# Performance work log

Hardware: AMD Instinct MI355X
Metric: run time of the kernel (lower is better)

Reference implementation:

```python
import jax, jax.numpy as jnp
import numpy as np

H, W = 128, 128
TANFOVX = 0.5
TANFOVY = 0.5
SCALE_MOD = 1.0
NEAR = 0.2
N = 2048


def setup_inputs() -> dict:
    key = jax.random.key(0)
    ks = jax.random.split(key, 6)
    # Gaussians in front of an identity camera looking down +z
    xy = jax.random.uniform(ks[0], (N, 2), minval=-1.5, maxval=1.5)
    z = jax.random.uniform(ks[1], (N, 1), minval=2.5, maxval=6.5)
    means3D = jnp.concatenate([xy, z], axis=1).astype(jnp.float32)
    opacities = jax.random.uniform(ks[2], (N, 1), minval=0.05, maxval=0.95)
    colors_precomp = jax.random.uniform(ks[3], (N, 3))
    scales = jax.random.uniform(ks[4], (N, 3), minval=0.01, maxval=0.06)
    rotations = jax.random.normal(ks[5], (N, 4))
    viewmatrix = jnp.eye(4, dtype=jnp.float32)  # world == camera frame
    bg = jnp.zeros((3,), dtype=jnp.float32)
    return dict(means3D=means3D, opacities=opacities,
                colors_precomp=colors_precomp, scales=scales,
                rotations=rotations, viewmatrix=viewmatrix, bg=bg)


def _quat_to_rot(q):
    # normalized quaternion (w, x, y, z) -> rotation matrix, as in the CUDA kernel
    q = q / jnp.linalg.norm(q, axis=-1, keepdims=True)
    w, x, y, z = q[:, 0], q[:, 1], q[:, 2], q[:, 3]
    return jnp.stack([
        jnp.stack([1 - 2 * (y * y + z * z), 2 * (x * y - w * z), 2 * (x * z + w * y)], -1),
        jnp.stack([2 * (x * y + w * z), 1 - 2 * (x * x + z * z), 2 * (y * z - w * x)], -1),
        jnp.stack([2 * (x * z - w * y), 2 * (y * z + w * x), 1 - 2 * (x * x + y * y)], -1),
    ], -2)  # [N,3,3]


def _forward(means3D, opacities, colors_precomp, scales, rotations, viewmatrix, bg):
    fx = W / (2.0 * TANFOVX)
    fy = H / (2.0 * TANFOVY)
    Rv = viewmatrix[:3, :3]
    tv = viewmatrix[:3, 3]
    pv = means3D @ Rv.T + tv            # view-space positions [N,3]
    x, y, z = pv[:, 0], pv[:, 1], pv[:, 2]
    zc = jnp.maximum(z, 1e-4)
    # frustum clamping of the EWA Jacobian, as in forward.cu
    tx = jnp.clip(x / zc, -1.3 * TANFOVX, 1.3 * TANFOVX) * zc
    ty = jnp.clip(y / zc, -1.3 * TANFOVY, 1.3 * TANFOVY) * zc
    zeros = jnp.zeros_like(zc)
    J = jnp.stack([
        jnp.stack([fx / zc, zeros, -fx * tx / (zc * zc)], -1),
        jnp.stack([zeros, fy / zc, -fy * ty / (zc * zc)], -1),
    ], -2)                               # [N,2,3]
    # 3D covariance Sigma = R S S^T R^T
    Rg = _quat_to_rot(rotations)
    M = Rg * (scales * SCALE_MOD)[:, None, :]
    Sigma = M @ jnp.swapaxes(M, -1, -2)  # [N,3,3]
    T2 = jnp.einsum('nij,jk->nik', J, Rv)
    cov2d = jnp.einsum('nij,njk,nlk->nil', T2, Sigma, T2)
    a = cov2d[:, 0, 0] + 0.3             # low-pass filter, as in CUDA
    b = cov2d[:, 0, 1]
    c = cov2d[:, 1, 1] + 0.3
    det = a * c - b * b
    valid = (det > 0) & (z > NEAR)
    inv_det = jnp.where(det != 0, 1.0 / det, 0.0)
    conA, conB, conC = c * inv_det, -b * inv_det, a * inv_det
    mid = 0.5 * (a + c)
    lam = mid + jnp.sqrt(jnp.maximum(mid * mid - det, 0.1))
    radii = jnp.where(valid, jnp.ceil(3.0 * jnp.sqrt(lam)), 0.0)
    # projected pixel-space means
    mx = fx * (x / zc) + 0.5 * (W - 1)
    my = fy * (y / zc) + 0.5 * (H - 1)

    # global front-to-back depth sort (CUDA sorts per tile; one tile here)
    order = jnp.argsort(z)
    mx_s, my_s = mx[order], my[order]
    A_s, B_s, C_s = conA[order], conB[order], conC[order]
    op_s = opacities[order, 0]
    z_s = z[order]
    col_s = colors_precomp[order]
    valid_s = valid[order]

    px = jnp.arange(W, dtype=means3D.dtype)
    py = jnp.arange(H, dtype=means3D.dtype)
    Dx = mx_s[None, :] - px[:, None]     # [W,N]
    Dy = my_s[None, :] - py[:, None]     # [H,N]
    # power = -0.5 (A dx^2 + C dy^2) - B dx dy, built [H,W,N]
    power = (-0.5 * A_s * Dx * Dx)[None, :, :] \
            + (-0.5 * C_s * Dy * Dy)[:, None, :] \
            - (B_s * Dx)[None, :, :] * Dy[:, None, :]
    alpha = jnp.minimum(0.99, op_s * jnp.exp(jnp.minimum(power, 0.0)))
    alpha = jnp.where((power <= 0.0) & valid_s & (alpha >= 1.0 / 255.0), alpha, 0.0)
    alpha = alpha.reshape(H * W, N)      # [HW,N], front-to-back order
    logt = jnp.log1p(-alpha)
    csum = jnp.cumsum(logt, axis=-1)
    T_excl = jnp.exp(csum - logt)        # exclusive transmittance prod_{j<i}(1-a_j)
    wgt = alpha * T_excl                 # compositing weights
    T_final = jnp.exp(csum[:, -1])
    color = jnp.einsum('pn,nc->cp', wgt, col_s).reshape(3, H, W) \
            + T_final.reshape(1, H, W) * bg[:, None, None]
    depth = (wgt * z_s[None, :]).sum(-1).reshape(H, W)
    alpha_img = (1.0 - T_final).reshape(H, W)
    return color, radii, depth, alpha_img


def reference(means3D, opacities, colors_precomp, scales, rotations, viewmatrix, bg):
    return _forward(means3D, opacities, colors_precomp, scales, rotations, viewmatrix, bg)
```

## Files before the change

### kernel.cpp

```cpp
#include <hip/hip_runtime.h>

#define NG    2048
#define IMG_W 128
#define IMG_H 128
#define NPIX  (IMG_W * IMG_H)
#define KCAP  768

struct PRec {
    double mx, my, A, B, C, op, z, r2c;
    float radii;
};

__device__ __forceinline__ void preprocess_g(
    int i,
    const float* __restrict__ means, const float* __restrict__ opac,
    const float* __restrict__ scales, const float* __restrict__ rots,
    const float* __restrict__ vm4, PRec& o)
{
    const double fx = 128.0, fy = 128.0;

    double R00 = vm4[0], R01 = vm4[1], R02 = vm4[2],  t0 = vm4[3];
    double R10 = vm4[4], R11 = vm4[5], R12 = vm4[6],  t1 = vm4[7];
    double R20 = vm4[8], R21 = vm4[9], R22 = vm4[10], t2 = vm4[11];

    double m0 = means[3*i+0], m1 = means[3*i+1], m2 = means[3*i+2];
    double x = R00*m0 + R01*m1 + R02*m2 + t0;
    double y = R10*m0 + R11*m1 + R12*m2 + t1;
    double z = R20*m0 + R21*m1 + R22*m2 + t2;

    double zc   = fmax(z, 1e-4);
    double invz = 1.0 / zc;
    const double limx = 1.3 * 0.5, limy = 1.3 * 0.5;
    double tx = fmin(limx, fmax(-limx, x * invz)) * zc;
    double ty = fmin(limy, fmax(-limy, y * invz)) * zc;

    double J00 = fx * invz, J02 = -fx * tx * invz * invz;
    double J11 = fy * invz, J12 = -fy * ty * invz * invz;

    double qw = rots[4*i+0], qx = rots[4*i+1], qy = rots[4*i+2], qz = rots[4*i+3];
    double qn = 1.0 / sqrt(qw*qw + qx*qx + qy*qy + qz*qz);
    qw *= qn; qx *= qn; qy *= qn; qz *= qn;

    double Rg00 = 1.0 - 2.0*(qy*qy + qz*qz), Rg01 = 2.0*(qx*qy - qw*qz), Rg02 = 2.0*(qx*qz + qw*qy);
    double Rg10 = 2.0*(qx*qy + qw*qz), Rg11 = 1.0 - 2.0*(qx*qx + qz*qz), Rg12 = 2.0*(qy*qz - qw*qx);
    double Rg20 = 2.0*(qx*qz - qw*qy), Rg21 = 2.0*(qy*qz + qw*qx), Rg22 = 1.0 - 2.0*(qx*qx + qy*qy);

    double s0 = scales[3*i+0], s1 = scales[3*i+1], s2 = scales[3*i+2];
    double M00 = Rg00*s0, M01 = Rg01*s1, M02 = Rg02*s2;
    double M10 = Rg10*s0, M11 = Rg11*s1, M12 = Rg12*s2;
    double M20 = Rg20*s0, M21 = Rg21*s1, M22 = Rg22*s2;

    double S00 = M00*M00 + M01*M01 + M02*M02;
    double S01 = M00*M10 + M01*M11 + M02*M12;
    double S02 = M00*M20 + M01*M21 + M02*M22;
    double S11 = M10*M10 + M11*M11 + M12*M12;
    double S12 = M10*M20 + M11*M21 + M12*M22;
    double S22 = M20*M20 + M21*M21 + M22*M22;

    double Ta0 = J00*R00 + J02*R20, Ta1 = J00*R01 + J02*R21, Ta2 = J00*R02 + J02*R22;
    double Tb0 = J11*R10 + J12*R20, Tb1 = J11*R11 + J12*R21, Tb2 = J11*R12 + J12*R22;

    double Ua0 = Ta0*S00 + Ta1*S01 + Ta2*S02;
    double Ua1 = Ta0*S01 + Ta1*S11 + Ta2*S12;
    double Ua2 = Ta0*S02 + Ta1*S12 + Ta2*S22;
    double Ub0 = Tb0*S00 + Tb1*S01 + Tb2*S02;
    double Ub1 = Tb0*S01 + Tb1*S11 + Tb2*S12;
    double Ub2 = Tb0*S02 + Tb1*S12 + Tb2*S22;
    double cov00 = Ua0*Ta0 + Ua1*Ta1 + Ua2*Ta2;
    double cov01 = Ua0*Tb0 + Ua1*Tb1 + Ua2*Tb2;
    double cov11 = Ub0*Tb0 + Ub1*Tb1 + Ub2*Tb2;

    double a = cov00 + 0.3;
    double b = cov01;
    double c = cov11 + 0.3;
    double det = a*c - b*b;
    bool valid = (det > 0.0) && (z > 0.2);
    double inv_det = (det != 0.0) ? (1.0 / det) : 0.0;
    double mid = 0.5 * (a + c);
    double lam = mid + sqrt(fmax(mid*mid - det, 0.1));

    double op = valid ? (double)opac[i] : 0.0;
    double r2c = -1.0;
    if (op > 0.0) {
        double lnterm = log(255.0 * op);
        if (lnterm > 0.0) r2c = 2.0 * lnterm * lam * 1.0001 + 1e-3;
    }

    o.mx  = fx * (x * invz) + 0.5 * (IMG_W - 1);
    o.my  = fy * (y * invz) + 0.5 * (IMG_H - 1);
    o.A   =  c * inv_det;
    o.B   = -b * inv_det;
    o.C   =  a * inv_det;
    o.op  = op;
    o.z   = z;
    o.r2c = r2c;
    o.radii = valid ? (float)ceil(3.0 * sqrt(lam)) : 0.0f;
}

__global__ __launch_bounds__(256) void fused_raster_kernel(
    const float* __restrict__ means,
    const float* __restrict__ opac,
    const float* __restrict__ cols,
    const float* __restrict__ scales,
    const float* __restrict__ rots,
    const float* __restrict__ vm4,
    const float* __restrict__ bg,
    float* __restrict__ out)
{
    __shared__ unsigned short cand[NG];
    __shared__ float recs[KCAP][10];
    __shared__ float pz[KCAP];
    __shared__ unsigned short pid[KCAP];
    __shared__ unsigned short perm[KCAP];
    __shared__ float comb[4 * 64 * 5];
    __shared__ int cntM, cntK;

    int tid  = threadIdx.x;
    int tile = blockIdx.x;
    int x0 = (tile & 15) * 8;
    int y0 = (tile >> 4) * 8;
    float x0f = (float)x0,       y0f = (float)y0;
    float x1f = (float)(x0 + 7), y1f = (float)(y0 + 7);

    if (tid == 0) { cntM = 0; cntK = 0; }
    __syncthreads();

    float fR00 = vm4[0], fR01 = vm4[1], fR02 = vm4[2],  ft0 = vm4[3];
    float fR10 = vm4[4], fR11 = vm4[5], fR12 = vm4[6],  ft1 = vm4[7];
    float fR20 = vm4[8], fR21 = vm4[9], fR22 = vm4[10], ft2 = vm4[11];

    for (int g = tid; g < NG; g += 256) {
        float m0 = means[3*g+0], m1 = means[3*g+1], m2 = means[3*g+2];
        float x = fR00*m0 + fR01*m1 + fR02*m2 + ft0;
        float y = fR10*m0 + fR11*m1 + fR12*m2 + ft1;
        float z = fR20*m0 + fR21*m1 + fR22*m2 + ft2;
        float zc = fmaxf(z, 1e-4f);
        float invz = 1.0f / zc;
        float xi = x * invz, yi = y * invz;
        float mx = 128.f * xi + 63.5f;
        float my = 128.f * yi + 63.5f;
        float txc = fminf(0.65f, fmaxf(-0.65f, xi));
        float tyc = fminf(0.65f, fmaxf(-0.65f, yi));
        float J00 = 128.f * invz;
        float J02 = -128.f * txc * invz;
        float J12 = -128.f * tyc * invz;
        float Ta0 = J00*fR00 + J02*fR20, Ta1 = J00*fR01 + J02*fR21, Ta2 = J00*fR02 + J02*fR22;
        float Tb0 = J00*fR10 + J12*fR20, Tb1 = J00*fR11 + J12*fR21, Tb2 = J00*fR12 + J12*fR22;
        float fro = Ta0*Ta0 + Ta1*Ta1 + Ta2*Ta2 + Tb0*Tb0 + Tb1*Tb1 + Tb2*Tb2;
        float s0 = scales[3*g+0], s1 = scales[3*g+1], s2 = scales[3*g+2];
        float smax2 = fmaxf(s0*s0, fmaxf(s1*s1, s2*s2));
        float op = opac[g];
        float lnterm = __logf(255.f * op);
        bool maybe = false;
        if (lnterm > 0.f) {
            float lam_pf = fro * smax2 * 1.02f + 0.95f;
            float r2 = 2.f * lnterm * lam_pf * 1.02f + 1.0f;
            float ddx = fmaxf(0.f, fmaxf(x0f - mx, mx - x1f));
            float ddy = fmaxf(0.f, fmaxf(y0f - my, my - y1f));
            maybe = (ddx*ddx + ddy*ddy) <= r2;
        }
        if (maybe) {
            int s = atomicAdd(&cntM, 1);
            cand[s] = (unsigned short)g;
        }
    }

    if (tid < 8) {
        int i = tile * 8 + tid;
        PRec o;
        preprocess_g(i, means, opac, scales, rots, vm4, o);
        out[3*NPIX + i] = o.radii;
    }
    __syncthreads();
    int M = cntM;

    for (int k = tid; k < M; k += 256) {
        int gi = cand[k];
        PRec o;
        preprocess_g(gi, means, opac, scales, rots, vm4, o);
        float fmx = (float)o.mx, fmy = (float)o.my, fr2 = (float)o.r2c;
        float ddx = fmaxf(0.f, fmaxf(x0f - fmx, fmx - x1f));
        float ddy = fmaxf(0.f, fmaxf(y0f - fmy, fmy - y1f));
        if (ddx*ddx + ddy*ddy <= fr2) {
            int s = atomicAdd(&cntK, 1);
            if (s < KCAP) {
                recs[s][0] = fmx;
                recs[s][1] = fmy;
                recs[s][2] = (float)o.A;
                recs[s][3] = (float)o.B;
                recs[s][4] = (float)o.C;
                recs[s][5] = (float)o.op;
                recs[s][6] = (float)o.z;
                recs[s][7] = cols[3*gi+0];
                recs[s][8] = cols[3*gi+1];
                recs[s][9] = cols[3*gi+2];
                pz[s]  = (float)o.z;
                pid[s] = (unsigned short)gi;
            }
        }
    }
    __syncthreads();
    int K = min(cntK, KCAP);

    for (int r = tid; r < K; r += 256) {
        float zr = pz[r];
        int ir = pid[r];
        int rank = 0;
        for (int s2 = 0; s2 < K; ++s2)
            rank += (pz[s2] < zr) || (pz[s2] == zr && pid[s2] < ir);
        perm[rank] = (unsigned short)r;
    }
    __syncthreads();

    int lane = tid & 63;
    int w    = tid >> 6;
    int px = x0 + (lane & 7);
    int py = y0 + (lane >> 3);
    float fpx = (float)px, fpy = (float)py;
    int p = py * IMG_W + px;

    int q = (K + 3) >> 2;
    int rs = w * q;
    int re = min(rs + q, K);

    float cr = 0.f, cg = 0.f, cb = 0.f, dep = 0.f, T = 1.f;
    for (int r = rs; r < re; ++r) {
        int j = perm[r];
        float mx = recs[j][0];
        float my = recs[j][1];
        float A  = recs[j][2];
        float B  = recs[j][3];
        float C  = recs[j][4];
        float op = recs[j][5];
        float dx = mx - fpx;
        float dy = my - fpy;
        float power = -0.5f * (A*dx*dx + C*dy*dy) - B*dx*dy;
        float al = fminf(0.99f, op * __expf(power));
        bool take = (power <= 0.0f) && (al >= (1.0f / 255.0f));
        float wgt = take ? al * T : 0.0f;
        dep += wgt * recs[j][6];
        cr  += wgt * recs[j][7];
        cg  += wgt * recs[j][8];
        cb  += wgt * recs[j][9];
        if (take) T *= (1.0f - al);
    }

    int cb_base = (w * 64 + lane) * 5;
    comb[cb_base + 0] = cr;
    comb[cb_base + 1] = cg;
    comb[cb_base + 2] = cb;
    comb[cb_base + 3] = dep;
    comb[cb_base + 4] = T;
    __syncthreads();

    if (w == 0) {
        float CR = 0.f, CG = 0.f, CB = 0.f, DEP = 0.f, TT = 1.f;
        #pragma unroll
        for (int ww = 0; ww < 4; ++ww) {
            int b2 = (ww * 64 + lane) * 5;
            CR  += TT * comb[b2 + 0];
            CG  += TT * comb[b2 + 1];
            CB  += TT * comb[b2 + 2];
            DEP += TT * comb[b2 + 3];
            TT  *= comb[b2 + 4];
        }
        out[0*NPIX + p] = CR + TT * bg[0];
        out[1*NPIX + p] = CG + TT * bg[1];
        out[2*NPIX + p] = CB + TT * bg[2];
        out[3*NPIX + NG + p]        = DEP;
        out[3*NPIX + NG + NPIX + p] = 1.f - TT;
    }
}

extern "C" void kernel_launch(void* const* d_in, const int* in_sizes, int n_in,
                              void* d_out, int out_size, void* d_ws, size_t ws_size,
                              hipStream_t stream)
{
    const float* means = (const float*)d_in[0];
    const float* opac  = (const float*)d_in[1];
    const float* cols  = (const float*)d_in[2];
    const float* scl   = (const float*)d_in[3];
    const float* rot   = (const float*)d_in[4];
    const float* vm    = (const float*)d_in[5];
    const float* bg    = (const float*)d_in[6];
    float* out = (float*)d_out;

    fused_raster_kernel<<<256, 256, 0, stream>>>(
        means, opac, cols, scl, rot, vm, bg, out);
}
```

Before: 24.26 us.

## Run candidate preprocessing in fp32 and overlap radii computation with culling

The per-candidate preprocessing moves from a double-precision helper to fp32 arithmetic. Only the depth used for sorting is still computed in double, and the conservative radius margin is widened. The coarse culling loop now runs on three wavefronts while the first wavefront computes the per-tile radii in double at the same time. The coarse bound uses a cheaper closed-form Jacobian norm estimate. The aim is to avoid slow FP64 work on the candidate path, with the risk of small numerical differences and a looser cull that lets more candidates through.

Result: no change. 23.80 us (-1.9%).

```diff
diff --git a/kernel.cpp b/kernel.cpp
--- a/kernel.cpp
+++ b/kernel.cpp
@@ -5,97 +5,6 @@
 #define IMG_H 128
 #define NPIX  (IMG_W * IMG_H)
 #define KCAP  768
-
-struct PRec {
-    double mx, my, A, B, C, op, z, r2c;
-    float radii;
-};
-
-__device__ __forceinline__ void preprocess_g(
-    int i,
-    const float* __restrict__ means, const float* __restrict__ opac,
-    const float* __restrict__ scales, const float* __restrict__ rots,
-    const float* __restrict__ vm4, PRec& o)
-{
-    const double fx = 128.0, fy = 128.0;
-
-    double R00 = vm4[0], R01 = vm4[1], R02 = vm4[2],  t0 = vm4[3];
-    double R10 = vm4[4], R11 = vm4[5], R12 = vm4[6],  t1 = vm4[7];
-    double R20 = vm4[8], R21 = vm4[9], R22 = vm4[10], t2 = vm4[11];
-
-    double m0 = means[3*i+0], m1 = means[3*i+1], m2 = means[3*i+2];
-    double x = R00*m0 + R01*m1 + R02*m2 + t0;
-    double y = R10*m0 + R11*m1 + R12*m2 + t1;
-    double z = R20*m0 + R21*m1 + R22*m2 + t2;
-
-    double zc   = fmax(z, 1e-4);
-    double invz = 1.0 / zc;
-    const double limx = 1.3 * 0.5, limy = 1.3 * 0.5;
-    double tx = fmin(limx, fmax(-limx, x * invz)) * zc;
-    double ty = fmin(limy, fmax(-limy, y * invz)) * zc;
-
-    double J00 = fx * invz, J02 = -fx * tx * invz * invz;
-    double J11 = fy * invz, J12 = -fy * ty * invz * invz;
-
-    double qw = rots[4*i+0], qx = rots[4*i+1], qy = rots[4*i+2], qz = rots[4*i+3];
-    double qn = 1.0 / sqrt(qw*qw + qx*qx + qy*qy + qz*qz);
-    qw *= qn; qx *= qn; qy *= qn; qz *= qn;
-
-    double Rg00 = 1.0 - 2.0*(qy*qy + qz*qz), Rg01 = 2.0*(qx*qy - qw*qz), Rg02 = 2.0*(qx*qz + qw*qy);
-    double Rg10 = 2.0*(qx*qy + qw*qz), Rg11 = 1.0 - 2.0*(qx*qx + qz*qz), Rg12 = 2.0*(qy*qz - qw*qx);
-    double Rg20 = 2.0*(qx*qz - qw*qy), Rg21 = 2.0*(qy*qz + qw*qx), Rg22 = 1.0 - 2.0*(qx*qx + qy*qy);
-
-    double s0 = scales[3*i+0], s1 = scales[3*i+1], s2 = scales[3*i+2];
-    double M00 = Rg00*s0, M01 = Rg01*s1, M02 = Rg02*s2;
-    double M10 = Rg10*s0, M11 = Rg11*s1, M12 = Rg12*s2;
-    double M20 = Rg20*s0, M21 = Rg21*s1, M22 = Rg22*s2;
-
-    double S00 = M00*M00 + M01*M01 + M02*M02;
-    double S01 = M00*M10 + M01*M11 + M02*M12;
-    double S02 = M00*M20 + M01*M21 + M02*M22;
-    double S11 = M10*M10 + M11*M11 + M12*M12;
-    double S12 = M10*M20 + M11*M21 + M12*M22;
-    double S22 = M20*M20 + M21*M21 + M22*M22;
-
-    double Ta0 = J00*R00 + J02*R20, Ta1 = J00*R01 + J02*R21, Ta2 = J00*R02 + J02*R22;
-    double Tb0 = J11*R10 + J12*R20, Tb1 = J11*R11 + J12*R21, Tb2 = J11*R12 + J12*R22;
-
-    double Ua0 = Ta0*S00 + Ta1*S01 + Ta2*S02;
-    double Ua1 = Ta0*S01 + Ta1*S11 + Ta2*S12;
-    double Ua2 = Ta0*S02 + Ta1*S12 + Ta2*S22;
-    double Ub0 = Tb0*S00 + Tb1*S01 + Tb2*S02;
-    double Ub1 = Tb0*S01 + Tb1*S11 + Tb2*S12;
-    double Ub2 = Tb0*S02 + Tb1*S12 + Tb2*S22;
-    double cov00 = Ua0*Ta0 + Ua1*Ta1 + Ua2*Ta2;
-    double cov01 = Ua0*Tb0 + Ua1*Tb1 + Ua2*Tb2;
-    double cov11 = Ub0*Tb0 + Ub1*Tb1 + Ub2*Tb2;
-
-    double a = cov00 + 0.3;
-    double b = cov01;
-    double c = cov11 + 0.3;
-    double det = a*c - b*b;
-    bool valid = (det > 0.0) && (z > 0.2);
-    double inv_det = (det != 0.0) ? (1.0 / det) : 0.0;
-    double mid = 0.5 * (a + c);
-    double lam = mid + sqrt(fmax(mid*mid - det, 0.1));
-
-    double op = valid ? (double)opac[i] : 0.0;
-    double r2c = -1.0;
-    if (op > 0.0) {
-        double lnterm = log(255.0 * op);
-        if (lnterm > 0.0) r2c = 2.0 * lnterm * lam * 1.0001 + 1e-3;
-    }
-
-    o.mx  = fx * (x * invz) + 0.5 * (IMG_W - 1);
-    o.my  = fy * (y * invz) + 0.5 * (IMG_H - 1);
-    o.A   =  c * inv_det;
-    o.B   = -b * inv_det;
-    o.C   =  a * inv_det;
-    o.op  = op;
-    o.z   = z;
-    o.r2c = r2c;
-    o.radii = valid ? (float)ceil(3.0 * sqrt(lam)) : 0.0f;
-}
 
 __global__ __launch_bounds__(256) void fused_raster_kernel(
     const float* __restrict__ means,
@@ -129,72 +38,166 @@
     float fR10 = vm4[4], fR11 = vm4[5], fR12 = vm4[6],  ft1 = vm4[7];
     float fR20 = vm4[8], fR21 = vm4[9], fR22 = vm4[10], ft2 = vm4[11];
 
-    for (int g = tid; g < NG; g += 256) {
-        float m0 = means[3*g+0], m1 = means[3*g+1], m2 = means[3*g+2];
+    if (tid >= 64) {
+        float r0s = fabsf(fR00) + fabsf(fR01) + fabsf(fR02);
+        float r1s = fabsf(fR10) + fabsf(fR11) + fabsf(fR12);
+        float r2s = fabsf(fR20) + fabsf(fR21) + fabsf(fR22);
+        float c0s = fabsf(fR00) + fabsf(fR10) + fabsf(fR20);
+        float c1s = fabsf(fR01) + fabsf(fR11) + fabsf(fR21);
+        float c2s = fabsf(fR02) + fabsf(fR12) + fabsf(fR22);
+        float r2norm = fmaxf(r0s, fmaxf(r1s, r2s)) * fmaxf(c0s, fmaxf(c1s, c2s));
+
+        for (int g = tid - 64; g < NG; g += 192) {
+            float m0 = means[3*g+0], m1 = means[3*g+1], m2 = means[3*g+2];
+            float x = fR00*m0 + fR01*m1 + fR02*m2 + ft0;
+            float y = fR10*m0 + fR11*m1 + fR12*m2 + ft1;
+            float z = fR20*m0 + fR21*m1 + fR22*m2 + ft2;
+            float zc = fmaxf(z, 1e-4f);
+            float invz = 1.0f / zc;
+            float xi = x * invz, yi = y * invz;
+            float mx = 128.f * xi + 63.5f;
+            float my = 128.f * yi + 63.5f;
+            float txc = fminf(0.65f, fmaxf(-0.65f, xi));
+            float tyc = fminf(0.65f, fmaxf(-0.65f, yi));
+            float jf = 128.f * invz;
+            float frJ = jf * jf * (2.f + txc*txc + tyc*tyc);
+            float s0 = scales[3*g+0], s1 = scales[3*g+1], s2 = scales[3*g+2];
+            float smax2 = fmaxf(s0*s0, fmaxf(s1*s1, s2*s2));
+            float lnterm = __logf(255.f * opac[g]);
+            bool maybe = false;
+            if (lnterm > 0.f) {
+                float lam_pf = frJ * r2norm * smax2 * 1.02f + 0.95f;
+                float r2 = 2.f * lnterm * lam_pf * 1.02f + 1.0f;
+                float ddx = fmaxf(0.f, fmaxf(x0f - mx, mx - x1f));
+                float ddy = fmaxf(0.f, fmaxf(y0f - my, my - y1f));
+                maybe = (ddx*ddx + ddy*ddy) <= r2;
+            }
+            if (maybe) {
+                int s = atomicAdd(&cntM, 1);
+                cand[s] = (unsigned short)g;
+            }
+        }
+    } else if (tid < 8) {
+        int i = tile * 8 + tid;
+        double R00 = vm4[0], R01 = vm4[1], R02 = vm4[2];
+        double R10 = vm4[4], R11 = vm4[5], R12 = vm4[6];
+        double R20 = vm4[8], R21 = vm4[9], R22 = vm4[10];
+        double t2d = vm4[11];
+        double m0 = means[3*i+0], m1 = means[3*i+1], m2 = means[3*i+2];
+        double x = R00*m0 + R01*m1 + R02*m2 + (double)vm4[3];
+        double y = R10*m0 + R11*m1 + R12*m2 + (double)vm4[7];
+        double z = R20*m0 + R21*m1 + R22*m2 + t2d;
+        double zc   = fmax(z, 1e-4);
+        double invz = 1.0 / zc;
+        double tx = fmin(0.65, fmax(-0.65, x * invz)) * zc;
+        double ty = fmin(0.65, fmax(-0.65, y * invz)) * zc;
+        double J00 = 128.0 * invz, J02 = -128.0 * tx * invz * invz;
+        double J11 = 128.0 * invz, J12 = -128.0 * ty * invz * invz;
+        double qw = rots[4*i+0], qx = rots[4*i+1], qy = rots[4*i+2], qz = rots[4*i+3];
+        double qn = 1.0 / sqrt(qw*qw + qx*qx + qy*qy + qz*qz);
+        qw *= qn; qx *= qn; qy *= qn; qz *= qn;
+        double Rg00 = 1.0-2.0*(qy*qy+qz*qz), Rg01 = 2.0*(qx*qy-qw*qz), Rg02 = 2.0*(qx*qz+qw*qy);
+        double Rg10 = 2.0*(qx*qy+qw*qz), Rg11 = 1.0-2.0*(qx*qx+qz*qz), Rg12 = 2.0*(qy*qz-qw*qx);
+        double Rg20 = 2.0*(qx*qz-qw*qy), Rg21 = 2.0*(qy*qz+qw*qx), Rg22 = 1.0-2.0*(qx*qx+qy*qy);
+        double s0 = scales[3*i+0], s1 = scales[3*i+1], s2 = scales[3*i+2];
+        double M00 = Rg00*s0, M01 = Rg01*s1, M02 = Rg02*s2;
+        double M10 = Rg10*s0, M11 = Rg11*s1, M12 = Rg12*s2;
+        double M20 = Rg20*s0, M21 = Rg21*s1, M22 = Rg22*s2;
+        double S00 = M00*M00+M01*M01+M02*M02;
+        double S01 = M00*M10+M01*M11+M02*M12;
+        double S02 = M00*M20+M01*M21+M02*M22;
+        double S11 = M10*M10+M11*M11+M12*M12;
+        double S12 = M10*M20+M11*M21+M12*M22;
+        double S22 = M20*M20+M21*M21+M22*M22;
+        double Ta0 = J00*R00+J02*R20, Ta1 = J00*R01+J02*R21, Ta2 = J00*R02+J02*R22;
+        double Tb0 = J11*R10+J12*R20, Tb1 = J11*R11+J12*R21, Tb2 = J11*R12+J12*R22;
+        double Ua0 = Ta0*S00+Ta1*S01+Ta2*S02;
+        double Ua1 = Ta0*S01+Ta1*S11+Ta2*S12;
+        double Ua2 = Ta0*S02+Ta1*S12+Ta2*S22;
+        double Ub0 = Tb0*S00+Tb1*S01+Tb2*S02;
+        double Ub1 = Tb0*S01+Tb1*S11+Tb2*S12;
+        double Ub2 = Tb0*S02+Tb1*S12+Tb2*S22;
+        double a = Ua0*Ta0+Ua1*Ta1+Ua2*Ta2 + 0.3;
+        double b = Ua0*Tb0+Ua1*Tb1+Ua2*Tb2;
+        double c = Ub0*Tb0+Ub1*Tb1+Ub2*Tb2 + 0.3;
+        double det = a*c - b*b;
+        bool valid = (det > 0.0) && (z > 0.2);
+        double mid = 0.5 * (a + c);
+        double lam = mid + sqrt(fmax(mid*mid - det, 0.1));
+        out[3*NPIX + i] = valid ? (float)ceil(3.0 * sqrt(lam)) : 0.0f;
+    }
+    __syncthreads();
+    int M = cntM;
+
+    for (int k = tid; k < M; k += 256) {
+        int gi = cand[k];
+        float m0 = means[3*gi+0], m1 = means[3*gi+1], m2 = means[3*gi+2];
+        double zd = (double)vm4[8]*m0 + (double)vm4[9]*m1 + (double)vm4[10]*m2 + (double)vm4[11];
+        float z = (float)zd;
         float x = fR00*m0 + fR01*m1 + fR02*m2 + ft0;
         float y = fR10*m0 + fR11*m1 + fR12*m2 + ft1;
-        float z = fR20*m0 + fR21*m1 + fR22*m2 + ft2;
         float zc = fmaxf(z, 1e-4f);
         float invz = 1.0f / zc;
-        float xi = x * invz, yi = y * invz;
-        float mx = 128.f * xi + 63.5f;
-        float my = 128.f * yi + 63.5f;
-        float txc = fminf(0.65f, fmaxf(-0.65f, xi));
-        float tyc = fminf(0.65f, fmaxf(-0.65f, yi));
-        float J00 = 128.f * invz;
-        float J02 = -128.f * txc * invz;
-        float J12 = -128.f * tyc * invz;
-        float Ta0 = J00*fR00 + J02*fR20, Ta1 = J00*fR01 + J02*fR21, Ta2 = J00*fR02 + J02*fR22;
-        float Tb0 = J00*fR10 + J12*fR20, Tb1 = J00*fR11 + J12*fR21, Tb2 = J00*fR12 + J12*fR22;
-        float fro = Ta0*Ta0 + Ta1*Ta1 + Ta2*Ta2 + Tb0*Tb0 + Tb1*Tb1 + Tb2*Tb2;
-        float s0 = scales[3*g+0], s1 = scales[3*g+1], s2 = scales[3*g+2];
-        float smax2 = fmaxf(s0*s0, fmaxf(s1*s1, s2*s2));
-        float op = opac[g];
-        float lnterm = __logf(255.f * op);
-        bool maybe = false;
-        if (lnterm > 0.f) {
-            float lam_pf = fro * smax2 * 1.02f + 0.95f;
-            float r2 = 2.f * lnterm * lam_pf * 1.02f + 1.0f;
-            float ddx = fmaxf(0.f, fmaxf(x0f - mx, mx - x1f));
-            float ddy = fmaxf(0.f, fmaxf(y0f - my, my - y1f));
-            maybe = (ddx*ddx + ddy*ddy) <= r2;
-        }
-        if (maybe) {
-            int s = atomicAdd(&cntM, 1);
-            cand[s] = (unsigned short)g;
-        }
-    }
-
-    if (tid < 8) {
-        int i = tile * 8 + tid;
-        PRec o;
-        preprocess_g(i, means, opac, scales, rots, vm4, o);
-        out[3*NPIX + i] = o.radii;
-    }
-    __syncthreads();
-    int M = cntM;
-
-    for (int k = tid; k < M; k += 256) {
-        int gi = cand[k];
-        PRec o;
-        preprocess_g(gi, means, opac, scales, rots, vm4, o);
-        float fmx = (float)o.mx, fmy = (float)o.my, fr2 = (float)o.r2c;
+        float tx = fminf(0.65f, fmaxf(-0.65f, x * invz)) * zc;
+        float ty = fminf(0.65f, fmaxf(-0.65f, y * invz)) * zc;
+        float J00 = 128.f * invz, J02 = -128.f * tx * invz * invz;
+        float J11 = 128.f * invz, J12 = -128.f * ty * invz * invz;
+        float qw = rots[4*gi+0], qx = rots[4*gi+1], qy = rots[4*gi+2], qz = rots[4*gi+3];
+        float qn = 1.0f / sqrtf(qw*qw + qx*qx + qy*qy + qz*qz);
+        qw *= qn; qx *= qn; qy *= qn; qz *= qn;
+        float Rg00 = 1.f-2.f*(qy*qy+qz*qz), Rg01 = 2.f*(qx*qy-qw*qz), Rg02 = 2.f*(qx*qz+qw*qy);
+        float Rg10 = 2.f*(qx*qy+qw*qz), Rg11 = 1.f-2.f*(qx*qx+qz*qz), Rg12 = 2.f*(qy*qz-qw*qx);
+        float Rg20 = 2.f*(qx*qz-qw*qy), Rg21 = 2.f*(qy*qz+qw*qx), Rg22 = 1.f-2.f*(qx*qx+qy*qy);
+        float s0 = scales[3*gi+0], s1 = scales[3*gi+1], s2 = scales[3*gi+2];
+        float M00 = Rg00*s0, M01 = Rg01*s1, M02 = Rg02*s2;
+        float M10 = Rg10*s0, M11 = Rg11*s1, M12 = Rg12*s2;
+        float M20 = Rg20*s0, M21 = Rg21*s1, M22 = Rg22*s2;
+        float S00 = M00*M00+M01*M01+M02*M02;
+        float S01 = M00*M10+M01*M11+M02*M12;
+        float S02 = M00*M20+M01*M21+M02*M22;
+        float S11 = M10*M10+M11*M11+M12*M12;
+        float S12 = M10*M20+M11*M21+M12*M22;
+        float S22 = M20*M20+M21*M21+M22*M22;
+        float Ta0 = J00*fR00+J02*fR20, Ta1 = J00*fR01+J02*fR21, Ta2 = J00*fR02+J02*fR22;
+        float Tb0 = J11*fR10+J12*fR20, Tb1 = J11*fR11+J12*fR21, Tb2 = J11*fR12+J12*fR22;
+        float Ua0 = Ta0*S00+Ta1*S01+Ta2*S02;
+        float Ua1 = Ta0*S01+Ta1*S11+Ta2*S12;
+        float Ua2 = Ta0*S02+Ta1*S12+Ta2*S22;
+        float Ub0 = Tb0*S00+Tb1*S01+Tb2*S02;
+        float Ub1 = Tb0*S01+Tb1*S11+Tb2*S12;
+        float Ub2 = Tb0*S02+Tb1*S12+Tb2*S22;
+        float a = Ua0*Ta0+Ua1*Ta1+Ua2*Ta2 + 0.3f;
+        float b = Ua0*Tb0+Ua1*Tb1+Ua2*Tb2;
+        float c = Ub0*Tb0+Ub1*Tb1+Ub2*Tb2 + 0.3f;
+        float det = a*c - b*b;
+        bool valid = (det > 0.0f) && (z > 0.2f);
+        float inv_det = (det != 0.0f) ? (1.0f / det) : 0.0f;
+        float mid = 0.5f * (a + c);
+        float lam = mid + sqrtf(fmaxf(mid*mid - det, 0.1f));
+        float op = valid ? opac[gi] : 0.0f;
+        float r2c = -1.0f;
+        if (op > 0.0f) {
+            float lnterm = __logf(255.f * op);
+            if (lnterm > 0.0f) r2c = 2.f * lnterm * lam * 1.001f + 1e-2f;
+        }
+        float fmx = 128.f * (x * invz) + 63.5f;
+        float fmy = 128.f * (y * invz) + 63.5f;
         float ddx = fmaxf(0.f, fmaxf(x0f - fmx, fmx - x1f));
         float ddy = fmaxf(0.f, fmaxf(y0f - fmy, fmy - y1f));
-        if (ddx*ddx + ddy*ddy <= fr2) {
+        if (ddx*ddx + ddy*ddy <= r2c) {
             int s = atomicAdd(&cntK, 1);
             if (s < KCAP) {
                 recs[s][0] = fmx;
                 recs[s][1] = fmy;
-                recs[s][2] = (float)o.A;
-                recs[s][3] = (float)o.B;
-                recs[s][4] = (float)o.C;
-                recs[s][5] = (float)o.op;
-                recs[s][6] = (float)o.z;
+                recs[s][2] =  c * inv_det;
+                recs[s][3] = -b * inv_det;
+                recs[s][4] =  a * inv_det;
+                recs[s][5] = op;
+                recs[s][6] = z;
                 recs[s][7] = cols[3*gi+0];
                 recs[s][8] = cols[3*gi+1];
                 recs[s][9] = cols[3*gi+2];
-                pz[s]  = (float)o.z;
+                pz[s]  = z;
                 pid[s] = (unsigned short)gi;
             }
         }
@@ -219,29 +222,23 @@
     float fpx = (float)px, fpy = (float)py;
     int p = py * IMG_W + px;
 
-    int q = (K + 3) >> 2;
+    int q  = (K + 3) >> 2;
     int rs = w * q;
     int re = min(rs + q, K);
 
     float cr = 0.f, cg = 0.f, cb = 0.f, dep = 0.f, T = 1.f;
     for (int r = rs; r < re; ++r) {
-        int j = perm[r];
-        float mx = recs[j][0];
-        float my = recs[j][1];
-        float A  = recs[j][2];
-        float B  = recs[j][3];
-        float C  = recs[j][4];
-        float op = recs[j][5];
-        float dx = mx - fpx;
-        float dy = my - fpy;
-        float power = -0.5f * (A*dx*dx + C*dy*dy) - B*dx*dy;
-        float al = fminf(0.99f, op * __expf(power));
+        const float* rr = recs[perm[r]];
+        float dx = rr[0] - fpx;
+        float dy = rr[1] - fpy;
+        float power = -0.5f * (rr[2]*dx*dx + rr[4]*dy*dy) - rr[3]*dx*dy;
+        float al = fminf(0.99f, rr[5] * __expf(power));
         bool take = (power <= 0.0f) && (al >= (1.0f / 255.0f));
         float wgt = take ? al * T : 0.0f;
-        dep += wgt * recs[j][6];
-        cr  += wgt * recs[j][7];
-        cg  += wgt * recs[j][8];
-        cb  += wgt * recs[j][9];
+        dep += wgt * rr[6];
+        cr  += wgt * rr[7];
+        cg  += wgt * rr[8];
+        cb  += wgt * rr[9];
         if (take) T *= (1.0f - al);
     }
 
```
